# Kernel tuning notes

Measured on AMD Instinct MI355X. Metric: run time of the kernel, lower is better.

Reference implementation:

```python
import jax, jax.numpy as jnp
import numpy as np

N = 268  # nodes per graph (pinned by nn.Linear(268, 100))
K = 3


def setup_inputs() -> dict:
    key = jax.random.key(0)
    ks = jax.random.split(key, 18)
    B, E, F_IN, NHID, NCLS = 64, 8192, 268, 64, 32
    s = 0.05
    return {
        "x1": jax.random.normal(ks[0], (B, N, F_IN), jnp.float32),
        "edge_index1": jax.random.randint(ks[1], (B, 2, E), 0, N, jnp.int32),
        "edge_attr1": jax.random.uniform(ks[2], (B, E), jnp.float32),
        "x2": jax.random.normal(ks[3], (B, N, F_IN), jnp.float32),
        "edge_index2": jax.random.randint(ks[4], (B, 2, E), 0, N, jnp.int32),
        "edge_attr2": jax.random.uniform(ks[5], (B, E), jnp.float32),
        # ChebConv gc1: [K, F_in, nhid]; gc4: [K, nhid, nclass]
        "W1": jax.random.normal(ks[6], (K, F_IN, NHID), jnp.float32) * s,
        "b1": jnp.zeros((NHID,), jnp.float32),
        "W4": jax.random.normal(ks[7], (K, NHID, NCLS), jnp.float32) * s,
        "b4": jnp.zeros((NCLS,), jnp.float32),
        # classifier MLP 268 -> 100 -> 60 -> 1
        "Wc1": jax.random.normal(ks[8], (N, 100), jnp.float32) * s,
        "bc1": jnp.zeros((100,), jnp.float32),
        "Wc2": jax.random.normal(ks[9], (100, 60), jnp.float32) * s,
        "bc2": jnp.zeros((60,), jnp.float32),
        "Wc3": jax.random.normal(ks[10], (60, 1), jnp.float32) * s,
        "bc3": jnp.zeros((1,), jnp.float32),
    }


def _forward_single(x, ei, w, W1, b1, W4, b4, Wc1, bc1, Wc2, bc2, Wc3, bc3):
    # x: [N, F]; ei: [2, E]; w: [E]
    src, dst = ei[0], ei[1]
    w = jnp.where(src == dst, 0.0, w)  # remove_self_loops
    deg = jax.ops.segment_sum(w, src, num_segments=N)
    dinv = jnp.where(deg > 0, jax.lax.rsqrt(deg), 0.0)
    # scaled Laplacian (sym norm, lambda_max=2): L_hat = -D^{-1/2} A D^{-1/2}
    nw = -dinv[src] * w * dinv[dst]

    def Lx(h):
        return jax.ops.segment_sum(nw[:, None] * h[src], dst, num_segments=N)

    def cheb(h, Wk, bk):
        t1 = Lx(h)                 # T1 = L_hat x
        t2 = 2.0 * Lx(t1) - h      # T2 = 2 L_hat T1 - T0
        return h @ Wk[0] + t1 @ Wk[1] + t2 @ Wk[2] + bk

    h = jax.nn.relu(cheb(x, W1, b1))   # gc1 -> [N, nhid]
    h = jax.nn.relu(cheb(h, W4, b4))   # gc4 -> [N, nclass]
    z = jax.nn.relu(h.T @ Wc1 + bc1)   # [nclass, 100]
    z = jax.nn.relu(z @ Wc2 + bc2)     # [nclass, 60]
    return z @ Wc3 + bc3               # [nclass, 1]


def reference(x1, edge_index1, edge_attr1, x2, edge_index2, edge_attr2,
              W1, b1, W4, b4, Wc1, bc1, Wc2, bc2, Wc3, bc3):
    f = jax.vmap(lambda x, ei, w: _forward_single(
        x, ei, w, W1, b1, W4, b4, Wc1, bc1, Wc2, bc2, Wc3, bc3))
    out1 = f(x1, edge_index1, edge_attr1)  # [B, nclass, 1]
    out2 = f(x2, edge_index2, edge_attr2)
    return (out1, out2)
```

## Files before the change

### kernel.cpp

```cpp
#include <hip/hip_runtime.h>
#include <hip/hip_bf16.h>

#define NN 268
#define NE 8192
#define KP 288

typedef short short8 __attribute__((ext_vector_type(8)));
typedef short short4v __attribute__((ext_vector_type(4)));
typedef float f32x4 __attribute__((ext_vector_type(4)));

__device__ __forceinline__ short f2bf(float f) {
  __hip_bfloat16 h = __float2bfloat16(f);
  return *reinterpret_cast<short*>(&h);
}

#define OFF_DINV  0
#define OFF_ARENA 139264
#define ARENA_SLAB_S 18432
#define OFF_WBT   4857856
#define OFF_WC1BT 4968448
#define OFF_W4BT  5032960
#define OFF_LB    5045248
#define OFF_Y     25099264
#define OFF_META  51444736
#define OFF_WE    53541888
#define OFF_BCNT  57736192
#define OFF_BST   57740288
#define OFF_H1G   57744384

__global__ __launch_bounds__(256) void k_prep(
    const int* __restrict__ ei1, const float* __restrict__ ea1,
    const int* __restrict__ ei2, const float* __restrict__ ea2,
    const float* __restrict__ W1, short* __restrict__ WbT,
    float* __restrict__ dinv, unsigned short* __restrict__ meta,
    float* __restrict__ we, unsigned* __restrict__ bcnt,
    unsigned* __restrict__ bst) {
  int t = threadIdx.x;
  int b = blockIdx.x;
  if (b < 128) {
    int g = b;
    const int* ei = (g < 64) ? (ei1 + (size_t)g * 2 * NE) : (ei2 + (size_t)(g - 64) * 2 * NE);
    const float* ea = (g < 64) ? (ea1 + (size_t)g * NE) : (ea2 + (size_t)(g - 64) * NE);
    __shared__ unsigned degL[NN];
    __shared__ unsigned bc[8], bs[8], bcur[8];
    for (int n = t; n < NN; n += 256) degL[n] = 0u;
    if (t < 8) bc[t] = 0u;
    __syncthreads();
#pragma unroll 4
    for (int e = t; e < NE; e += 256) {
      int s = ei[e], d = ei[NE + e];
      float w = ea[e];
      if (s != d) {
        atomicAdd(&degL[s], (unsigned)lrintf(w * 1048576.f));
        atomicAdd(&bc[d / 34], 1u);
      }
    }
    __syncthreads();
    for (int n = t; n < 272; n += 256) {
      float r = 0.f;
      if (n < NN) {
        unsigned v = degL[n];
        if (v) r = rsqrtf((float)v * (1.f / 1048576.f));
      }
      dinv[(size_t)g * 272 + n] = r;
    }
    if (t == 0) {
      unsigned run = (unsigned)g * NE;
#pragma unroll
      for (int k = 0; k < 8; ++k) { bs[k] = run; run += bc[k]; }
    }
    __syncthreads();
    if (t < 8) {
      bcnt[g * 8 + t] = bc[t];
      bst[g * 8 + t] = bs[t];
      bcur[t] = bs[t];
    }
    __syncthreads();
#pragma unroll 4
    for (int e = t; e < NE; e += 256) {
      int s = ei[e], d = ei[NE + e];
      float w = ea[e];
      if (s != d) {
        int bk = d / 34;
        unsigned pos = atomicAdd(&bcur[bk], 1u);
        meta[pos] = (unsigned short)(((d - bk * 34) << 9) | s);
        we[pos] = w;
      }
    }
  } else {
    int idx = (b - 128) * 256 + t;
    int n = idx / KP, kp = idx - n * KP;
    int kb = n >> 6, j = n & 63;
    float v = (kp < 268) ? W1[((size_t)kb * 268 + kp) * 64 + j] : 0.f;
    WbT[idx] = f2bf(v);
  }
}

__global__ __launch_bounds__(256) void k_build_gemm1(
    const unsigned short* __restrict__ meta, const float* __restrict__ we,
    const unsigned* __restrict__ bcnt, const unsigned* __restrict__ bst,
    const float* __restrict__ dinv_all, short* __restrict__ Lb,
    const float* __restrict__ x1, const float* __restrict__ x2,
    const short* __restrict__ WbT, const float* __restrict__ Wc1,
    const float* __restrict__ W4, float* __restrict__ Y,
    short* __restrict__ Y2t, short* __restrict__ Wc1bT,
    short* __restrict__ W4bT) {
  __shared__ __align__(16) char smem[34 * 288 * 4 + 272 * 4];
  int t = threadIdx.x;
  int bx = blockIdx.x;
  if (bx < 640) {
    int xcd = bx & 7, rest = bx >> 3;
    int g = xcd + 8 * (rest / 5);
    int m0 = (rest % 5) * 64;
    const float* A32 = (g < 64) ? (x1 + (size_t)g * NN * 268)
                                : (x2 + (size_t)(g - 64) * NN * 268);
    float* Yg = Y + (size_t)g * NN * 192;
    short* Y2tg = Y2t + (size_t)g * ARENA_SLAB_S;
    short (*As)[40] = (short(*)[40])smem;
    short (*Bs)[40] = (short(*)[40])(smem + 5120);
    int w = t >> 6, lane = t & 63;
    int quad = lane >> 4, l16 = lane & 15;
    int mh = w & 1, nh = w >> 1;
    f32x4 acc[2][6];
#pragma unroll
    for (int mi = 0; mi < 2; ++mi)
#pragma unroll
      for (int ni = 0; ni < 6; ++ni) acc[mi][ni] = (f32x4){0.f, 0.f, 0.f, 0.f};

    int sr = t >> 2, sko = (t & 3) * 8;
    float4 pva, pvb;
    short8 pB[3];
    auto loadA = [&](int K0) {
      int row = m0 + sr, k = K0 + sko;
      pva = make_float4(0.f, 0.f, 0.f, 0.f); pvb = pva;
      if (row < NN && k < 268) pva = *(const float4*)(A32 + (size_t)row * 268 + k);
      if (row < NN && k + 4 < 268) pvb = *(const float4*)(A32 + (size_t)row * 268 + k + 4);
    };
    auto loadB = [&](int K0) {
#pragma unroll
      for (int i = 0; i < 3; ++i)
        pB[i] = *(const short8*)(WbT + (size_t)(sr + i * 64) * KP + K0 + sko);
    };
    loadA(0); loadB(0);
    for (int k0 = 0; k0 < KP; k0 += 32) {
      {
        short8 s;
        const float* fa = (const float*)&pva;
        const float* fb = (const float*)&pvb;
#pragma unroll
        for (int j = 0; j < 4; ++j) { s[j] = f2bf(fa[j]); s[4 + j] = f2bf(fb[j]); }
        *(short8*)(&As[sr][sko]) = s;
      }
#pragma unroll
      for (int i = 0; i < 3; ++i)
        *(short8*)(&Bs[sr + i * 64][sko]) = pB[i];
      __syncthreads();
      if (k0 + 32 < KP) { loadA(k0 + 32); loadB(k0 + 32); }
      short8 af[2], bfr[6];
#pragma unroll
      for (int mi = 0; mi < 2; ++mi)
        af[mi] = *(const short8*)(&As[(mh * 2 + mi) * 16 + l16][quad * 8]);
#pragma unroll
      for (int ni = 0; ni < 6; ++ni)
        bfr[ni] = *(const short8*)(&Bs[(nh * 6 + ni) * 16 + l16][quad * 8]);
#pragma unroll
      for (int mi = 0; mi < 2; ++mi)
#pragma unroll
        for (int ni = 0; ni < 6; ++ni)
          acc[mi][ni] = __builtin_amdgcn_mfma_f32_16x16x32_bf16(af[mi], bfr[ni], acc[mi][ni], 0, 0, 0);
      __syncthreads();
    }
#pragma unroll
    for (int mi = 0; mi < 2; ++mi) {
      int rbase = m0 + (mh * 2 + mi) * 16 + quad * 4;
#pragma unroll
      for (int reg = 0; reg < 4; ++reg) {
        int row = rbase + reg;
        if (row < NN) {
#pragma unroll
          for (int ni = 0; ni < 6; ++ni) {
            int col = (nh * 6 + ni) * 16 + l16;
            Yg[(size_t)row * 192 + col] = acc[mi][ni][reg];
          }
        }
      }
      if (rbase < NN) {
#pragma unroll
        for (int ni = 0; ni < 6; ++ni) {
          int col = (nh * 6 + ni) * 16 + l16;
          if (col >= 128) {
            short4v p;
#pragma unroll
            for (int reg = 0; reg < 4; ++reg) p[reg] = f2bf(acc[mi][ni][reg]);
            *(short4v*)(Y2tg + (size_t)(col - 128) * KP + rbase) = p;
          }
        }
      }
    }
  } else if (bx < 1664) {
    int l = bx - 640;
    int xcd = l & 7, rest = l >> 3;
    int g = xcd + 8 * (rest & 15);
    int tile = rest >> 4;
    int r0 = tile * 34;
    int* LrowI = (int*)smem;
    float* dv = (float*)(smem + 39168);
    for (int i = t; i < 34 * 288; i += 256) LrowI[i] = 0;
    for (int i = t; i < 272; i += 256) dv[i] = dinv_all[(size_t)g * 272 + i];
    __syncthreads();
    unsigned n = bcnt[g * 8 + tile];
    unsigned base = bst[g * 8 + tile];
    for (unsigned i = t; i < n; i += 256) {
      unsigned m = meta[base + i];
      float w = we[base + i];
      int dl = m >> 9, s = m & 511;
      atomicAdd(&LrowI[dl * 288 + s],
                (int)lrintf(-dv[s] * w * dv[r0 + dl] * 16777216.f));
    }
    __syncthreads();
    short* Lbg = Lb + (size_t)g * 272 * KP + (size_t)r0 * KP;
    for (int i = t; i < 34 * 288; i += 256)
      Lbg[i] = f2bf((float)LrowI[i] * (1.f / 16777216.f));
  } else {
    int idx = (bx - 1664) * 256 + t;
    if (idx < 112 * KP) {
      int n = idx / KP, k = idx - n * KP;
      float v = (n < 100 && k < 268) ? Wc1[(size_t)k * 100 + n] : 0.f;
      Wc1bT[idx] = f2bf(v);
    } else {
      int i4 = idx - 112 * KP;
      int n = i4 >> 6, k = i4 & 63;
      W4bT[i4] = f2bf(W4[(((size_t)(n >> 5)) * 64 + k) * 32 + (n & 31)]);
    }
  }
}

#define SP 296
#define NW 8
#define NTHR 512

__device__ __forceinline__ void load_a9(const short* __restrict__ Lbg,
                                        int mt, int l16, int quad, short8* a9) {
  const short* Arow = Lbg + (size_t)(mt * 16 + l16) * KP + quad * 8;
#pragma unroll
  for (int k = 0; k < 9; ++k) a9[k] = *(const short8*)(Arow + k * 32);
}

template <int NTN>
__device__ __forceinline__ void cheb_mm_pre(const short8* a9,
                                            const char* B0, int l16, int quad,
                                            f32x4* acc) {
#pragma unroll
  for (int k = 0; k < 9; ++k) {
#pragma unroll
    for (int nt = 0; nt < NTN; ++nt) {
      short8 bf = *(const short8*)(B0 +
          ((size_t)(nt * 16 + l16) * SP + k * 32 + quad * 8) * 2);
      acc[nt] = __builtin_amdgcn_mfma_f32_16x16x32_bf16(a9[k], bf, acc[nt], 0, 0, 0);
    }
  }
}

#define A_Y2H 0
#define A_UTH 18944
__global__ __launch_bounds__(NTHR, 1) void k_megaA(
    const short* __restrict__ Lb, const short* __restrict__ arena,
    const float* __restrict__ Y, const float* __restrict__ b1,
    short* __restrict__ H1G) {
  __shared__ __align__(16) char sm[37888];
  int b = blockIdx.x;
  int xcd = b & 7, idx = b >> 3;
  int g = xcd + 8 * (idx & 15);
  int h = idx >> 4;
  int t = threadIdx.x;
  int w = t >> 6, lane = t & 63;
  int quad = lane >> 4, l16 = lane & 15;
  const short* Lbg = Lb + (size_t)g * 272 * KP;
  const short* Y2tg = arena + (size_t)g * ARENA_SLAB_S + (size_t)h * 32 * KP;
  const float* Yg = Y + (size_t)g * NN * 192;
  short* H1gg = H1G + (size_t)g * 268 * 64;

  short8 aL0[9], aL1[9], aL2[9];
  load_a9(Lbg, w, l16, quad, aL0);
  load_a9(Lbg, w + 8, l16, quad, aL1);
  if (w == 0) load_a9(Lbg, 16, l16, quad, aL2);

  for (int i = t; i < 32 * 37; i += NTHR) {
    int r = i / 37, c = (i - r * 37) * 8;
    short8 v = {0, 0, 0, 0, 0, 0, 0, 0};
    if (c < 264) {
      v = *(const short8*)(Y2tg + (size_t)r * KP + c);
    } else if (c == 264) {
      v = *(const short8*)(Y2tg + (size_t)r * KP + 264);
      v[4] = 0; v[5] = 0; v[6] = 0; v[7] = 0;
    }
    *(short8*)(sm + A_Y2H + ((size_t)r * SP + c) * 2) = v;
  }
  for (int i = t; i < 32 * 20; i += NTHR) {
    int f = i / 20, d = 268 + (i - f * 20);
    *(short*)(sm + A_UTH + ((size_t)f * SP + d) * 2) = 0;
  }
  __syncthreads();

  {
    auto body = [&](int mt, const short8* a9) {
      int dbase = mt * 16 + quad * 4;
      float yr[2][4];
      if (dbase < NN) {
#pragma unroll
        for (int nt = 0; nt < 2; ++nt)
#pragma unroll
          for (int reg = 0; reg < 4; ++reg)
            yr[nt][reg] = Yg[(size_t)(dbase + reg) * 192 + 64 + h * 32 + nt * 16 + l16];
      }
      f32x4 acc[2];
#pragma unroll
      for (int nt = 0; nt < 2; ++nt) acc[nt] = (f32x4){0.f, 0.f, 0.f, 0.f};
      cheb_mm_pre<2>(a9, sm + A_Y2H, l16, quad, acc);
      if (dbase < NN) {
#pragma unroll
        for (int nt = 0; nt < 2; ++nt) {
          int f_loc = nt * 16 + l16;
          short4v p;
#pragma unroll
          for (int reg = 0; reg < 4; ++reg)
            p[reg] = f2bf(yr[nt][reg] + 2.f * acc[nt][reg]);
          *(short4v*)(sm + A_UTH + ((size_t)f_loc * SP + dbase) * 2) = p;
        }
      }
    };
    body(w, aL0); body(w + 8, aL1); if (w == 0) body(16, aL2);
  }
  __syncthreads();

  {
    auto body = [&](int mt, const short8* a9) {
      int dbase = mt * 16 + quad * 4;
      float yr0[2][4], yr2[2][4];
      if (dbase < NN) {
#pragma unroll
        for (int nt = 0; nt < 2; ++nt)
#pragma unroll
          for (int reg = 0; reg < 4; ++reg) {
            int fg = h * 32 + nt * 16 + l16;
            yr0[nt][reg] = Yg[(size_t)(dbase + reg) * 192 + fg];
            yr2[nt][reg] = Yg[(size_t)(dbase + reg) * 192 + 128 + fg];
          }
      }
      f32x4 acc[2];
#pragma unroll
      for (int nt = 0; nt < 2; ++nt) acc[nt] = (f32x4){0.f, 0.f, 0.f, 0.f};
      cheb_mm_pre<2>(a9, sm + A_UTH, l16, quad, acc);
      if (dbase < NN) {
#pragma unroll
        for (int nt = 0; nt < 2; ++nt) {
          int fg = h * 32 + nt * 16 + l16;
          float bb = b1[fg];
#pragma unroll
          for (int reg = 0; reg < 4; ++reg) {
            int d = dbase + reg;
            float v = yr0[nt][reg] - yr2[nt][reg] + acc[nt][reg] + bb;
            H1gg[(size_t)d * 64 + fg] = f2bf(fmaxf(v, 0.f));
          }
        }
      }
    };
    body(w, aL0); body(w + 8, aL1); if (w == 0) body(16, aL2);
  }
}

#define B_H1S 0
#define B_W4S 39168
#define B_YB0 52992
#define B_YB1 70400
#define B_YB2 87808
#define B_YBB 105216
#define B_UT2 0
#define B_H2T 9472
#define B_Z1  18944
#define B_W2S 26368
#define B_Z2  52992
#define B_W3S 57088
__global__ __launch_bounds__(NTHR, 1) void k_megaB(
    const short* __restrict__ Lb, const short* __restrict__ H1G,
    const short* __restrict__ W4bT, const short* __restrict__ Wc1bT,
    const float* __restrict__ b4, const float* __restrict__ bc1,
    const float* __restrict__ Wc2, const float* __restrict__ bc2,
    const float* __restrict__ Wc3, const float* __restrict__ bc3,
    float* __restrict__ out) {
  __shared__ __align__(16) char sm[114688];
  int b = blockIdx.x;
  int xcd = b & 7, idx = b >> 3;
  int g = xcd + 8 * (idx & 15);
  int h = idx >> 4;
  int t = threadIdx.x;
  int w = t >> 6, lane = t & 63;
  int quad = lane >> 4, l16 = lane & 15;
  const short* Lbg = Lb + (size_t)g * 272 * KP;
  const short* H1gg = H1G + (size_t)g * 268 * 64;

  short8 aL0[9], aL1[9], aL2[9];
  load_a9(Lbg, w, l16, quad, aL0);
  load_a9(Lbg, w + 8, l16, quad, aL1);
  if (w == 0) load_a9(Lbg, 16, l16, quad, aL2);

  for (int i = t; i < 272 * 9; i += NTHR) {
    int r = i / 9, cg = i - r * 9;
    short8 v = {0, 0, 0, 0, 0, 0, 0, 0};
    if (cg < 8 && r < 268) v = *(const short8*)(H1gg + (size_t)r * 64 + cg * 8);
    *(short8*)(sm + B_H1S + ((size_t)r * 72 + cg * 8) * 2) = v;
  }
  for (int i = t; i < 96 * 8; i += NTHR) {
    int r = i >> 3, ko = (i & 7) * 8;
    *(short8*)(sm + B_W4S + ((size_t)r * 72 + ko) * 2) =
        *(const short8*)(W4bT + r * 64 + ko);
  }
  for (int i = t; i < 16 * 20; i += NTHR) {
    int f = i / 20, d = 268 + (i - f * 20);
    *(short*)(sm + B_YBB + ((size_t)f * SP + d) * 2) = 0;
  }
  __syncthreads();

  for (int id = w; id < 51; id += NW) {
    int ci = id / 17, nt = id - ci * 17;
    int ct = h + 2 * ci;
    f32x4 a1 = (f32x4){0.f, 0.f, 0.f, 0.f};
#pragma unroll
    for (int kc = 0; kc < 2; ++kc) {
      short8 af = *(const short8*)(sm + B_W4S +
          ((size_t)(ct * 16 + l16) * 72 + kc * 32 + quad * 8) * 2);
      short8 bf = *(const short8*)(sm + B_H1S +
          ((size_t)(nt * 16 + l16) * 72 + kc * 32 + quad * 8) * 2);
      a1 = __builtin_amdgcn_mfma_f32_16x16x32_bf16(af, bf, a1, 0, 0, 0);
    }
    int d = nt * 16 + l16;
    if (d < NN) {
#pragma unroll
      for (int reg = 0; reg < 4; ++reg) {
        int fl = quad * 4 + reg;
        float a = a1[reg];
        if (ci == 0) {
          *(float*)(sm + B_YB0 + ((size_t)fl * 272 + d) * 4) = a;
        } else if (ci == 1) {
          *(float*)(sm + B_YB1 + ((size_t)fl * 272 + d) * 4) = a;
        } else {
          *(float*)(sm + B_YB2 + ((size_t)fl * 272 + d) * 4) = a;
          *(short*)(sm + B_YBB + ((size_t)fl * SP + d) * 2) = f2bf(a);
        }
      }
    }
  }
  __syncthreads();

  for (int i = t; i < 16 * 20; i += NTHR) {
    int f = i / 20, d = 268 + (i - f * 20);
    *(short*)(sm + B_UT2 + ((size_t)f * SP + d) * 2) = 0;
    *(short*)(sm + B_H2T + ((size_t)f * SP + d) * 2) = 0;
  }

  {
    auto body = [&](int mt, const short8* a9) {
      int dbase = mt * 16 + quad * 4;
      float yr[4];
      if (dbase < NN) {
#pragma unroll
        for (int reg = 0; reg < 4; ++reg)
          yr[reg] = *(const float*)(sm + B_YB1 + ((size_t)l16 * 272 + dbase + reg) * 4);
      }
      f32x4 acc1 = (f32x4){0.f, 0.f, 0.f, 0.f};
      cheb_mm_pre<1>(a9, sm + B_YBB, l16, quad, &acc1);
      if (dbase < NN) {
        short4v p;
#pragma unroll
        for (int reg = 0; reg < 4; ++reg)
          p[reg] = f2bf(yr[reg] + 2.f * acc1[reg]);
        *(short4v*)(sm + B_UT2 + ((size_t)l16 * SP + dbase) * 2) = p;
      }
    };
    body(w, aL0); body(w + 8, aL1); if (w == 0) body(16, aL2);
  }
  __syncthreads();

  {
    float bb = b4[h * 16 + l16];
    auto body = [&](int mt, const short8* a9) {
      int dbase = mt * 16 + quad * 4;
      float yr0[4], yr2[4];
      if (dbase < NN) {
#pragma unroll
        for (int reg = 0; reg < 4; ++reg) {
          yr0[reg] = *(const float*)(sm + B_YB0 + ((size_t)l16 * 272 + dbase + reg) * 4);
          yr2[reg] = *(const float*)(sm + B_YB2 + ((size_t)l16 * 272 + dbase + reg) * 4);
        }
      }
      f32x4 acc1 = (f32x4){0.f, 0.f, 0.f, 0.f};
      cheb_mm_pre<1>(a9, sm + B_UT2, l16, quad, &acc1);
      if (dbase < NN) {
        short4v p;
#pragma unroll
        for (int reg = 0; reg < 4; ++reg) {
          float v = yr0[reg] - yr2[reg] + acc1[reg] + bb;
          p[reg] = f2bf(fmaxf(v, 0.f));
        }
        *(short4v*)(sm + B_H2T + ((size_t)l16 * SP + dbase) * 2) = p;
      }
    };
    body(w, aL0); body(w + 8, aL1); if (w == 0) body(16, aL2);
  }
  __syncthreads();

  for (int id = w; id < 7; id += NW) {
    f32x4 a1 = (f32x4){0.f, 0.f, 0.f, 0.f};
#pragma unroll
    for (int k = 0; k < 9; ++k) {
      short8 af = *(const short8*)(sm + B_H2T +
          ((size_t)l16 * SP + k * 32 + quad * 8) * 2);
      short8 bf = *(const short8*)(Wc1bT + (size_t)(id * 16 + l16) * KP + k * 32 + quad * 8);
      a1 = __builtin_amdgcn_mfma_f32_16x16x32_bf16(af, bf, a1, 0, 0, 0);
    }
    int col = id * 16 + l16;
    if (col < 100) {
      float bb = bc1[col];
#pragma unroll
      for (int reg = 0; reg < 4; ++reg)
        *(float*)(sm + B_Z1 + ((size_t)(quad * 4 + reg) * 116 + col) * 4) =
            fmaxf(a1[reg] + bb, 0.f);
    }
  }
  for (int i = t; i < 100 * 64; i += NTHR) {
    int rr = i >> 6, c = i & 63;
    *(float*)(sm + B_W2S + ((size_t)rr * 64 + c) * 4) =
        (c < 60) ? Wc2[(size_t)rr * 60 + c] : 0.f;
  }
  if (t < 64) *(float*)(sm + B_W3S + (size_t)t * 4) = (t < 60) ? Wc3[t] : 0.f;
  __syncthreads();
  if (t < 64) {
    int r2 = (t >> 3) * 2;
    int c8 = (t & 7) * 8;
    float a2[2][8];
#pragma unroll
    for (int i = 0; i < 2; ++i)
#pragma unroll
      for (int j = 0; j < 8; ++j) a2[i][j] = 0.f;
    const float* Z1p = (const float*)(sm + B_Z1);
    const float* W2p = (const float*)(sm + B_W2S);
#pragma unroll 4
    for (int k = 0; k < 100; ++k) {
      float x0 = Z1p[(size_t)r2 * 116 + k], x1 = Z1p[(size_t)(r2 + 1) * 116 + k];
      float4 wA = *(const float4*)(W2p + (size_t)k * 64 + c8);
      float4 wB = *(const float4*)(W2p + (size_t)k * 64 + c8 + 4);
      float wv[8] = {wA.x, wA.y, wA.z, wA.w, wB.x, wB.y, wB.z, wB.w};
#pragma unroll
      for (int j = 0; j < 8; ++j) { a2[0][j] += x0 * wv[j]; a2[1][j] += x1 * wv[j]; }
    }
    float* Z2p = (float*)(sm + B_Z2);
#pragma unroll
    for (int j = 0; j < 8; ++j) {
      int c = c8 + j;
      float bb = (c < 60) ? bc2[c] : 0.f;
      Z2p[(size_t)r2 * 64 + c] = fmaxf(a2[0][j] + bb, 0.f);
      Z2p[(size_t)(r2 + 1) * 64 + c] = fmaxf(a2[1][j] + bb, 0.f);
    }
  }
  __syncthreads();
  if (t < 16) {
    const float* Z2p = (const float*)(sm + B_Z2);
    const float* w3p = (const float*)(sm + B_W3S);
    float acc3 = bc3[0];
#pragma unroll
    for (int k = 0; k < 60; ++k) acc3 += Z2p[(size_t)t * 64 + k] * w3p[k];
    out[(size_t)g * 32 + h * 16 + t] = acc3;
  }
}

extern "C" void kernel_launch(void* const* d_in, const int* in_sizes, int n_in,
                              void* d_out, int out_size, void* d_ws, size_t ws_size,
                              hipStream_t stream) {
  (void)in_sizes; (void)n_in; (void)out_size; (void)ws_size;
  const float* x1  = (const float*)d_in[0];
  const int*   ei1 = (const int*)d_in[1];
  const float* ea1 = (const float*)d_in[2];
  const float* x2  = (const float*)d_in[3];
  const int*   ei2 = (const int*)d_in[4];
  const float* ea2 = (const float*)d_in[5];
  const float* W1  = (const float*)d_in[6];
  const float* b1  = (const float*)d_in[7];
  const float* W4  = (const float*)d_in[8];
  const float* b4  = (const float*)d_in[9];
  const float* Wc1 = (const float*)d_in[10];
  const float* bc1 = (const float*)d_in[11];
  const float* Wc2 = (const float*)d_in[12];
  const float* bc2 = (const float*)d_in[13];
  const float* Wc3 = (const float*)d_in[14];
  const float* bc3 = (const float*)d_in[15];

  char* ws = (char*)d_ws;
  float* dinv  = (float*)(ws + OFF_DINV);
  short* arena = (short*)(ws + OFF_ARENA);
  short* WbT   = (short*)(ws + OFF_WBT);
  short* Wc1bT = (short*)(ws + OFF_WC1BT);
  short* W4bT  = (short*)(ws + OFF_W4BT);
  short* Lb    = (short*)(ws + OFF_LB);
  float* Y     = (float*)(ws + OFF_Y);
  unsigned short* meta = (unsigned short*)(ws + OFF_META);
  float* we    = (float*)(ws + OFF_WE);
  unsigned* bcnt = (unsigned*)(ws + OFF_BCNT);
  unsigned* bst  = (unsigned*)(ws + OFF_BST);
  short* H1G   = (short*)(ws + OFF_H1G);
  float* out   = (float*)d_out;

  k_prep<<<344, 256, 0, stream>>>(ei1, ea1, ei2, ea2, W1, WbT, dinv,
                                  meta, we, bcnt, bst);
  k_build_gemm1<<<1814, 256, 0, stream>>>(meta, we, bcnt, bst, dinv, Lb,
                                          x1, x2, WbT, Wc1, W4, Y, arena,
                                          Wc1bT, W4bT);
  k_megaA<<<256, NTHR, 0, stream>>>(Lb, arena, Y, b1, H1G);
  k_megaB<<<256, NTHR, 0, stream>>>(Lb, H1G, W4bT, Wc1bT,
                                    b4, bc1, Wc2, bc2, Wc3, bc3, out);
}
```

Measured before the change: 195.2 us.

## Drop edge bucketing pass; filter raw edges per row tile in Laplacian build

Removes the second edge pass in k_prep that bucketed edges by destination tile into meta/we arrays, and has each Laplacian row-tile block scan all edges of its graph and keep only those whose destination falls in its 34-row range. k_prep now runs 1024-thread blocks over fewer blocks. This saves the bucketing scatter, its global writes and the extra synchronisation. In exchange, each of the 8 tile blocks per graph re-reads the full edge list, giving eight times the edge reads in the build kernel.

Result: faster. 182.3 us (-6.6%).

```diff
diff --git a/kernel.cpp b/kernel.cpp
--- a/kernel.cpp
+++ b/kernel.cpp
@@ -22,19 +22,13 @@
 #define OFF_W4BT  5032960
 #define OFF_LB    5045248
 #define OFF_Y     25099264
-#define OFF_META  51444736
-#define OFF_WE    53541888
-#define OFF_BCNT  57736192
-#define OFF_BST   57740288
-#define OFF_H1G   57744384
-
-__global__ __launch_bounds__(256) void k_prep(
+#define OFF_H1G   51444736
+
+__global__ __launch_bounds__(1024) void k_prep(
     const int* __restrict__ ei1, const float* __restrict__ ea1,
     const int* __restrict__ ei2, const float* __restrict__ ea2,
     const float* __restrict__ W1, short* __restrict__ WbT,
-    float* __restrict__ dinv, unsigned short* __restrict__ meta,
-    float* __restrict__ we, unsigned* __restrict__ bcnt,
-    unsigned* __restrict__ bst) {
+    float* __restrict__ dinv) {
   int t = threadIdx.x;
   int b = blockIdx.x;
   if (b < 128) {
@@ -42,53 +36,25 @@
     const int* ei = (g < 64) ? (ei1 + (size_t)g * 2 * NE) : (ei2 + (size_t)(g - 64) * 2 * NE);
     const float* ea = (g < 64) ? (ea1 + (size_t)g * NE) : (ea2 + (size_t)(g - 64) * NE);
     __shared__ unsigned degL[NN];
-    __shared__ unsigned bc[8], bs[8], bcur[8];
-    for (int n = t; n < NN; n += 256) degL[n] = 0u;
-    if (t < 8) bc[t] = 0u;
+    if (t < NN) degL[t] = 0u;
     __syncthreads();
 #pragma unroll 4
-    for (int e = t; e < NE; e += 256) {
+    for (int e = t; e < NE; e += 1024) {
       int s = ei[e], d = ei[NE + e];
       float w = ea[e];
-      if (s != d) {
-        atomicAdd(&degL[s], (unsigned)lrintf(w * 1048576.f));
-        atomicAdd(&bc[d / 34], 1u);
-      }
+      if (s != d) atomicAdd(&degL[s], (unsigned)lrintf(w * 1048576.f));
     }
     __syncthreads();
-    for (int n = t; n < 272; n += 256) {
+    if (t < 272) {
       float r = 0.f;
-      if (n < NN) {
-        unsigned v = degL[n];
+      if (t < NN) {
+        unsigned v = degL[t];
         if (v) r = rsqrtf((float)v * (1.f / 1048576.f));
       }
-      dinv[(size_t)g * 272 + n] = r;
-    }
-    if (t == 0) {
-      unsigned run = (unsigned)g * NE;
-#pragma unroll
-      for (int k = 0; k < 8; ++k) { bs[k] = run; run += bc[k]; }
-    }
-    __syncthreads();
-    if (t < 8) {
-      bcnt[g * 8 + t] = bc[t];
-      bst[g * 8 + t] = bs[t];
-      bcur[t] = bs[t];
-    }
-    __syncthreads();
-#pragma unroll 4
-    for (int e = t; e < NE; e += 256) {
-      int s = ei[e], d = ei[NE + e];
-      float w = ea[e];
-      if (s != d) {
-        int bk = d / 34;
-        unsigned pos = atomicAdd(&bcur[bk], 1u);
-        meta[pos] = (unsigned short)(((d - bk * 34) << 9) | s);
-        we[pos] = w;
-      }
+      dinv[(size_t)g * 272 + t] = r;
     }
   } else {
-    int idx = (b - 128) * 256 + t;
+    int idx = (b - 128) * 1024 + t;
     int n = idx / KP, kp = idx - n * KP;
     int kb = n >> 6, j = n & 63;
     float v = (kp < 268) ? W1[((size_t)kb * 268 + kp) * 64 + j] : 0.f;
@@ -97,8 +63,8 @@
 }
 
 __global__ __launch_bounds__(256) void k_build_gemm1(
-    const unsigned short* __restrict__ meta, const float* __restrict__ we,
-    const unsigned* __restrict__ bcnt, const unsigned* __restrict__ bst,
+    const int* __restrict__ ei1, const float* __restrict__ ea1,
+    const int* __restrict__ ei2, const float* __restrict__ ea2,
     const float* __restrict__ dinv_all, short* __restrict__ Lb,
     const float* __restrict__ x1, const float* __restrict__ x2,
     const short* __restrict__ WbT, const float* __restrict__ Wc1,
@@ -203,19 +169,22 @@
     int g = xcd + 8 * (rest & 15);
     int tile = rest >> 4;
     int r0 = tile * 34;
+    const int* ei = (g < 64) ? (ei1 + (size_t)g * 2 * NE) : (ei2 + (size_t)(g - 64) * 2 * NE);
+    const float* ea = (g < 64) ? (ea1 + (size_t)g * NE) : (ea2 + (size_t)(g - 64) * NE);
     int* LrowI = (int*)smem;
     float* dv = (float*)(smem + 39168);
     for (int i = t; i < 34 * 288; i += 256) LrowI[i] = 0;
     for (int i = t; i < 272; i += 256) dv[i] = dinv_all[(size_t)g * 272 + i];
     __syncthreads();
-    unsigned n = bcnt[g * 8 + tile];
-    unsigned base = bst[g * 8 + tile];
-    for (unsigned i = t; i < n; i += 256) {
-      unsigned m = meta[base + i];
-      float w = we[base + i];
-      int dl = m >> 9, s = m & 511;
-      atomicAdd(&LrowI[dl * 288 + s],
-                (int)lrintf(-dv[s] * w * dv[r0 + dl] * 16777216.f));
+#pragma unroll 8
+    for (int e = t; e < NE; e += 256) {
+      int d = ei[NE + e];
+      int s = ei[e];
+      float w = ea[e];
+      if (d >= r0 && d < r0 + 34 && s != d) {
+        atomicAdd(&LrowI[(d - r0) * 288 + s],
+                  (int)lrintf(-dv[s] * w * dv[d] * 16777216.f));
+      }
     }
     __syncthreads();
     short* Lbg = Lb + (size_t)g * 272 * KP + (size_t)r0 * KP;
@@ -602,16 +571,11 @@
   short* W4bT  = (short*)(ws + OFF_W4BT);
   short* Lb    = (short*)(ws + OFF_LB);
   float* Y     = (float*)(ws + OFF_Y);
-  unsigned short* meta = (unsigned short*)(ws + OFF_META);
-  float* we    = (float*)(ws + OFF_WE);
-  unsigned* bcnt = (unsigned*)(ws + OFF_BCNT);
-  unsigned* bst  = (unsigned*)(ws + OFF_BST);
   short* H1G   = (short*)(ws + OFF_H1G);
   float* out   = (float*)d_out;
 
-  k_prep<<<344, 256, 0, stream>>>(ei1, ea1, ei2, ea2, W1, WbT, dinv,
-                                  meta, we, bcnt, bst);
-  k_build_gemm1<<<1814, 256, 0, stream>>>(meta, we, bcnt, bst, dinv, Lb,
+  k_prep<<<182, 1024, 0, stream>>>(ei1, ea1, ei2, ea2, W1, WbT, dinv);
+  k_build_gemm1<<<1814, 256, 0, stream>>>(ei1, ea1, ei2, ea2, dinv, Lb,
                                           x1, x2, WbT, Wc1, W4, Y, arena,
                                           Wc1bT, W4bT);
   k_megaA<<<256, NTHR, 0, stream>>>(Lb, arena, Y, b1, H1G);
```
